# Optimization experiments

Hardware: AMD Instinct MI355X
Metric: run time of the kernel (lower is better)

## Reference

```python
import jax, jax.numpy as jnp
import numpy as np

L = 32768      # sequence length
H = 512        # n_features == d_model
P = 128        # state_size // 2 (conj_sym)
EPS = 1e-5     # haiku LayerNorm default eps


def setup_inputs() -> dict:
    key = jax.random.key(0)
    ks = jax.random.split(key, 10)
    x = jax.random.normal(ks[0], (L, H), dtype=jnp.float32)
    # S5 parameters (HiPPO-like init approximated with random values of same structure)
    lambda_real = -(0.1 + 0.5 * jax.random.uniform(ks[1], (P,), dtype=jnp.float32))
    lambda_imag = jnp.pi * jnp.arange(P, dtype=jnp.float32)
    b = jax.random.normal(ks[2], (P, H, 2), dtype=jnp.float32) / np.sqrt(H)
    c = jax.random.normal(ks[3], (H, P, 2), dtype=jnp.float32) / np.sqrt(2 * P)
    d = jax.random.normal(ks[4], (H,), dtype=jnp.float32)
    # log-uniform timescales in [1e-3, 1e-1]
    u = jax.random.uniform(ks[5], (P, 1), dtype=jnp.float32)
    delta = jnp.log(1e-3) + u * (jnp.log(1e-1) - jnp.log(1e-3))
    norm_scale = jnp.ones((H,), dtype=jnp.float32)
    norm_offset = jnp.zeros((H,), dtype=jnp.float32)
    w2 = jax.random.normal(ks[6], (H, H), dtype=jnp.float32) / np.sqrt(H)
    b2 = jnp.zeros((H,), dtype=jnp.float32)
    return {"x": x, "lambda_real": lambda_real, "lambda_imag": lambda_imag,
            "b": b, "c": c, "d": d, "delta": delta,
            "norm_scale": norm_scale, "norm_offset": norm_offset,
            "w2": w2, "b2": b2}


def _s5_block(x, lambda_real, lambda_imag, b, c, d, delta, norm_scale, norm_offset, w2, b2):
    skip = x
    # prenorm LayerNorm over last axis
    mean = jnp.mean(x, axis=-1, keepdims=True)
    var = jnp.var(x, axis=-1, keepdims=True)
    xn = (x - mean) * jax.lax.rsqrt(var + EPS) * norm_scale + norm_offset

    # --- S5 SSM ---
    lam = lambda_real + 1j * lambda_imag                      # [P]
    B = b[..., 0] + 1j * b[..., 1]                            # [P, H]
    C = c[..., 0] + 1j * c[..., 1]                            # [H, P]
    step = jnp.exp(delta[:, 0])                               # [P] (step_rescale = 1)
    # bilinear discretization
    bl = 1.0 / (1.0 - (step / 2.0) * lam)
    lam_bar = bl * (1.0 + (step / 2.0) * lam)                 # [P]
    B_bar = (bl * step)[:, None] * B                          # [P, H]

    Bu = jnp.einsum('lh,ph->lp', xn.astype(jnp.complex64), B_bar)  # [L, P]
    lam_elems = jnp.broadcast_to(lam_bar, (L, P))

    def binop(qi, qj):
        Ai, bi = qi
        Aj, bj = qj
        return Aj * Ai, Aj * bi + bj

    _, xs = jax.lax.associative_scan(binop, (lam_elems, Bu))  # states [L, P]
    # conj_sym: output is 2 * Re(C x)
    ys = 2.0 * jnp.einsum('lp,hp->lh', xs, C).real            # [L, H]
    y = ys + d * xn                                           # D skip term

    # half_glu2 (dropout_rate = 0 -> identity)
    x1 = jax.nn.gelu(y)
    out = y * jax.nn.sigmoid(x1 @ w2 + b2)
    return skip + out


def reference(x, lambda_real, lambda_imag, b, c, d, delta, norm_scale, norm_offset, w2, b2):
    return _s5_block(x, lambda_real, lambda_imag, b, c, d, delta,
                     norm_scale, norm_offset, w2, b2)
```

## Files before the change

### kernel.cpp

```cpp
#include <hip/hip_runtime.h>
#include <hip/hip_bf16.h>
#include <math.h>

#define LSEQ 32768
#define HF   512
#define PS   128
#define TWOP 256
#define NC   512
#define CL   64

typedef __attribute__((ext_vector_type(8))) short short8v;
typedef __attribute__((ext_vector_type(4))) float f32x4;

__device__ __forceinline__ float sig_fast(float z) {
    return __builtin_amdgcn_rcpf(1.0f + __expf(-z));
}
__device__ __forceinline__ float gelu_fast(float v) {
    float z = 1.5957691216057308f * v * fmaf(0.044715f, v * v, 1.0f);
    return v * sig_fast(z);
}
__device__ __forceinline__ unsigned short bf16bits(float f) {
    __hip_bfloat16 h = __float2bfloat16(f);
    return *(unsigned short*)&h;
}
__device__ __forceinline__ float bf2f(unsigned short u) {
    unsigned v = ((unsigned)u) << 16;
    return *(float*)&v;
}
__device__ __forceinline__ unsigned pk2(float a, float b) {
    return ((unsigned)bf16bits(b) << 16) | bf16bits(a);
}
__device__ __forceinline__ void gload_lds16(const void* g, void* l) {
    __builtin_amdgcn_global_load_lds(
        (const __attribute__((address_space(1))) unsigned int*)g,
        (__attribute__((address_space(3))) unsigned int*)l, 16, 0, 0);
}
__device__ __forceinline__ void wait_vm0_barrier() {
    asm volatile("s_waitcnt vmcnt(0)" ::: "memory");
    __builtin_amdgcn_s_barrier();
}

__global__ __launch_bounds__(128) void prep_lam_k(
    const float* __restrict__ lr_, const float* __restrict__ li_,
    const float* __restrict__ delta, float* lam, float* bls, float* lamPow)
{
    int p = threadIdx.x;
    float lr = lr_[p], li = li_[p];
    float step = expf(delta[p]);
    float s2 = 0.5f * step;
    float dr = 1.0f - s2 * lr, di = -s2 * li;
    float inv = 1.0f / (dr * dr + di * di);
    float blr = dr * inv, bli = -di * inv;
    float nr = 1.0f + s2 * lr, ni = s2 * li;
    float lbr = blr * nr - bli * ni;
    float lbi = blr * ni + bli * nr;
    lam[2 * p] = lbr; lam[2 * p + 1] = lbi;
    bls[2 * p] = blr * step; bls[2 * p + 1] = bli * step;
    float pr = 1.0f, pim = 0.0f;
    lamPow[2 * p] = 1.0f; lamPow[2 * p + 1] = 0.0f;
    for (int k = 1; k <= CL; k++) {
        float t = pr * lbr - pim * lbi;
        pim = pr * lbi + pim * lbr;
        pr = t;
        lamPow[k * TWOP + 2 * p] = pr;
        lamPow[k * TWOP + 2 * p + 1] = pim;
    }
}

__global__ __launch_bounds__(256) void prep_B_k(
    const float* __restrict__ b, const float* __restrict__ bls,
    unsigned short* __restrict__ bwt)
{
    int idx = blockIdx.x * 256 + threadIdx.x;
    int p = idx >> 9, h = idx & 511;
    float2 bb = *(const float2*)(b + ((size_t)p * HF + h) * 2);
    float sr = bls[2 * p], si = bls[2 * p + 1];
    bwt[(size_t)(2 * p) * HF + h]     = bf16bits(sr * bb.x - si * bb.y);
    bwt[(size_t)(2 * p + 1) * HF + h] = bf16bits(sr * bb.y + si * bb.x);
}

__global__ __launch_bounds__(256) void prep_C_k(
    const float* __restrict__ c, unsigned short* __restrict__ cwt)
{
    int idx = blockIdx.x * 256 + threadIdx.x;
    int h = idx >> 7, p = idx & 127;
    float2 cc = *(const float2*)(c + ((size_t)h * PS + p) * 2);
    *(unsigned*)(cwt + (size_t)h * TWOP + 2 * p) = pk2(2.0f * cc.x, -2.0f * cc.y);
}

__global__ __launch_bounds__(256) void prep_w2_k(
    const float* __restrict__ w2, unsigned short* __restrict__ w2t)
{
    int idx = blockIdx.x * 256 + threadIdx.x;
    int n = idx >> 9, k = idx & 511;
    w2t[(size_t)n * HF + k] = bf16bits(w2[(size_t)k * HF + n]);
}

__global__ __launch_bounds__(128) void ln_k(
    const float* __restrict__ x, const float* __restrict__ scale,
    const float* __restrict__ offs, unsigned short* __restrict__ xnbf)
{
    int row = blockIdx.x, t = threadIdx.x;
    const float4* xr = (const float4*)(x + (size_t)row * HF);
    float4 v = xr[t];
    float s = v.x + v.y + v.z + v.w;
    float q = v.x * v.x + v.y * v.y + v.z * v.z + v.w * v.w;
    #pragma unroll
    for (int off = 32; off > 0; off >>= 1) {
        s += __shfl_down(s, off);
        q += __shfl_down(q, off);
    }
    __shared__ float ss[2], qq[2];
    if ((t & 63) == 0) { ss[t >> 6] = s; qq[t >> 6] = q; }
    __syncthreads();
    float S = ss[0] + ss[1], Q = qq[0] + qq[1];
    float mean = S * (1.0f / HF);
    float var = Q * (1.0f / HF) - mean * mean;
    float rstd = rsqrtf(var + 1e-5f);
    float4 sc = ((const float4*)scale)[t];
    float4 of = ((const float4*)offs)[t];
    ushort4 hv;
    hv.x = bf16bits((v.x - mean) * rstd * sc.x + of.x);
    hv.y = bf16bits((v.y - mean) * rstd * sc.y + of.y);
    hv.z = bf16bits((v.z - mean) * rstd * sc.z + of.z);
    hv.w = bf16bits((v.w - mean) * rstd * sc.w + of.w);
    ((ushort4*)(xnbf + (size_t)row * HF))[t] = hv;
}

__global__ __launch_bounds__(256) void g1scan_k(
    const unsigned short* __restrict__ A,
    const unsigned short* __restrict__ Bt,
    unsigned short* __restrict__ xs16,
    float* __restrict__ F,
    const float* __restrict__ lam)
{
    __shared__ float yt[128 * 128];
    unsigned short* Sb = (unsigned short*)yt;
    const int K = HF;
    int flat = (blockIdx.y << 1) + blockIdx.x;
    int f2 = (flat & 7) * 64 + (flat >> 3);
    const int bxi = f2 & 1, byi = f2 >> 1;
    const int bm = byi << 7;
    const int bn = bxi << 7;
    const int tid = threadIdx.x;
    const int lane = tid & 63;
    const int wid = tid >> 6;
    const int wr = wid >> 1, wc = wid & 1;

    f32x4 acc[4][4] = {};

    const int r0 = (wid << 5) + (lane >> 2);
    const int c0 = (lane & 3) << 3;
    const unsigned short* gA = A + (size_t)(bm + r0) * K + c0;
    const unsigned short* gB = Bt + (size_t)(bn + r0) * K + c0;
    const int stA0 = (wid << 5) * 32;
    const int stA1 = ((wid << 5) + 16) * 32;
    const int aoff = ((wr << 6) + (lane & 15)) * 32 + ((lane >> 4) << 3);
    const int boff = ((wc << 6) + (lane & 15)) * 32 + ((lane >> 4) << 3);

    #define G1_STAGE(b, k0) do { \
        gload_lds16(gA + (k0), Sb + (b) * 8192 + stA0); \
        gload_lds16(gA + (k0) + (size_t)16 * K, Sb + (b) * 8192 + stA1); \
        gload_lds16(gB + (k0), Sb + (b) * 8192 + 4096 + stA0); \
        gload_lds16(gB + (k0) + (size_t)16 * K, Sb + (b) * 8192 + 4096 + stA1); \
    } while (0)
    #define G1_COMPUTE(b) do { \
        short8v a_[4], b_[4]; \
        _Pragma("unroll") \
        for (int m = 0; m < 4; m++) \
            a_[m] = *(const short8v*)(Sb + (b) * 8192 + aoff + (m << 4) * 32); \
        _Pragma("unroll") \
        for (int n = 0; n < 4; n++) \
            b_[n] = *(const short8v*)(Sb + (b) * 8192 + 4096 + boff + (n << 4) * 32); \
        _Pragma("unroll") \
        for (int m = 0; m < 4; m++) \
            _Pragma("unroll") \
            for (int n = 0; n < 4; n++) \
                acc[m][n] = __builtin_amdgcn_mfma_f32_16x16x32_bf16( \
                    a_[m], b_[n], acc[m][n], 0, 0, 0); \
    } while (0)

    G1_STAGE(0, 0);
    wait_vm0_barrier();
    #pragma unroll
    for (int t = 0; t < 16; ++t) {
        const int cur = t & 1;
        if (t + 1 < 16) G1_STAGE(cur ^ 1, (t + 1) << 5);
        G1_COMPUTE(cur);
        wait_vm0_barrier();
    }

    #pragma unroll
    for (int m = 0; m < 4; m++) {
        const int rowb = (wr << 6) + (m << 4) + ((lane >> 4) << 2);
        #pragma unroll
        for (int n = 0; n < 4; n++) {
            const int col = (wc << 6) + (n << 4) + (lane & 15);
            #pragma unroll
            for (int j = 0; j < 4; j++)
                yt[(rowb + j) * 128 + col] = acc[m][n][j];
        }
    }
    __syncthreads();

    if (tid < 128) {
        int ch = tid >> 6, q = tid & 63;
        int pg = (bxi << 6) + q;
        float lr = lam[2 * pg], liv = lam[2 * pg + 1];
        float sr = 0.0f, si = 0.0f;
        float* col = yt + (ch << 6) * 128 + 2 * q;
        #pragma unroll 8
        for (int i = 0; i < CL; i++) {
            float ur = col[i * 128], ui = col[i * 128 + 1];
            float tr = lr * sr - liv * si + ur;
            float ti = lr * si + liv * sr + ui;
            sr = tr; si = ti;
            col[i * 128] = sr; col[i * 128 + 1] = si;
        }
        int cg = (byi << 1) + ch;
        F[(size_t)cg * TWOP + (bxi << 7) + 2 * q] = sr;
        F[(size_t)cg * TWOP + (bxi << 7) + 2 * q + 1] = si;
    }
    __syncthreads();

    #pragma unroll
    for (int j = 0; j < 8; j++) {
        int fl = j * 256 + tid;
        int r = fl >> 4, ck = fl & 15;
        float4 v0 = *(float4*)&yt[r * 128 + ck * 8];
        float4 v1 = *(float4*)&yt[r * 128 + ck * 8 + 4];
        uint4 o;
        o.x = pk2(v0.x, v0.y); o.y = pk2(v0.z, v0.w);
        o.z = pk2(v1.x, v1.y); o.w = pk2(v1.z, v1.w);
        *(uint4*)(xs16 + (size_t)(bm + r) * TWOP + bn + ck * 8) = o;
    }
}

__global__ __launch_bounds__(512) void carry_k(
    const float* __restrict__ F, float* __restrict__ G,
    const float* __restrict__ lamPow)
{
    __shared__ float2 buf[NC];
    int c = threadIdx.x, p = blockIdx.x;
    float2 f = *(const float2*)(F + (size_t)c * TWOP + 2 * p);
    buf[c] = f;
    float aR = lamPow[CL * TWOP + 2 * p], aI = lamPow[CL * TWOP + 2 * p + 1];
    __syncthreads();
    #pragma unroll
    for (int d = 1; d < NC; d <<= 1) {
        bool act = (c >= d);
        float2 pv = act ? buf[c - d] : make_float2(0.0f, 0.0f);
        __syncthreads();
        if (act) {
            float2 cur = buf[c];
            cur.x += aR * pv.x - aI * pv.y;
            cur.y += aR * pv.y + aI * pv.x;
            buf[c] = cur;
        }
        __syncthreads();
        float nR = aR * aR - aI * aI;
        float nI = 2.0f * aR * aI;
        aR = nR; aI = nI;
    }
    *(float2*)(G + (size_t)c * TWOP + 2 * p) = buf[c];
}

__global__ __launch_bounds__(128) void fix_k(
    const unsigned short* __restrict__ xs16, const float* __restrict__ G,
    const float* __restrict__ lamPow, unsigned short* __restrict__ xsbf)
{
    int bc = blockIdx.x;
    int c = bc >> 2, qq = bc & 3;
    int p = threadIdx.x;
    float gr = 0.0f, gi = 0.0f;
    if (c > 0) {
        float2 g = *(const float2*)(G + (size_t)(c - 1) * TWOP + 2 * p);
        gr = g.x; gi = g.y;
    }
    size_t base = ((size_t)c * CL + (qq << 4)) * TWOP + 2 * p;
    #pragma unroll
    for (int i = 0; i < 16; i++) {
        float2 lp = *(const float2*)(lamPow + (size_t)((qq << 4) + i + 1) * TWOP + 2 * p);
        unsigned u = *(const unsigned*)(xs16 + base + (size_t)i * TWOP);
        float vr = bf2f((unsigned short)(u & 0xffff)) + lp.x * gr - lp.y * gi;
        float vi = bf2f((unsigned short)(u >> 16))    + lp.x * gi + lp.y * gr;
        *(unsigned*)(xsbf + base + (size_t)i * TWOP) = pk2(vr, vi);
    }
}

template<int MODE, int KT, int NT>
__global__ __launch_bounds__(256) void mgemm_k(
    const unsigned short* __restrict__ A, const unsigned short* __restrict__ Bt,
    const float* __restrict__ e0, const unsigned short* __restrict__ e1h,
    const float* __restrict__ e2, float* __restrict__ outF,
    unsigned short* __restrict__ o1, unsigned short* __restrict__ o2)
{
    __shared__ float smem[8192];
    unsigned short* Sb = (unsigned short*)smem;
    float* eb = smem;

    constexpr int GX = NT >> 7;
    int flat = blockIdx.y * GX + blockIdx.x;
    constexpr int NWG = GX * (LSEQ >> 7);
    int f2 = (flat & 7) * (NWG >> 3) + (flat >> 3);
    const int bm = (f2 / GX) << 7;
    const int bn = (f2 % GX) << 7;

    const int tid = threadIdx.x;
    const int lane = tid & 63;
    const int wid = tid >> 6;
    const int wr = wid >> 1, wc = wid & 1;

    f32x4 acc[4][4] = {};

    const int r0 = (wid << 5) + (lane >> 2);
    const int c0 = (lane & 3) << 3;
    const unsigned short* gA = A + (size_t)(bm + r0) * KT + c0;
    const unsigned short* gB = Bt + (size_t)(bn + r0) * KT + c0;
    const int stA0 = (wid << 5) * 32;
    const int stA1 = ((wid << 5) + 16) * 32;
    const int aoff = ((wr << 6) + (lane & 15)) * 32 + ((lane >> 4) << 3);
    const int boff = ((wc << 6) + (lane & 15)) * 32 + ((lane >> 4) << 3);
    constexpr int NSTEP = KT >> 5;

    #define MG_STAGE(b, k0) do { \
        gload_lds16(gA + (k0), Sb + (b) * 8192 + stA0); \
        gload_lds16(gA + (k0) + (size_t)16 * KT, Sb + (b) * 8192 + stA1); \
        gload_lds16(gB + (k0), Sb + (b) * 8192 + 4096 + stA0); \
        gload_lds16(gB + (k0) + (size_t)16 * KT, Sb + (b) * 8192 + 4096 + stA1); \
    } while (0)
    #define MG_COMPUTE(b) do { \
        short8v a_[4], b_[4]; \
        _Pragma("unroll") \
        for (int m = 0; m < 4; m++) \
            a_[m] = *(const short8v*)(Sb + (b) * 8192 + aoff + (m << 4) * 32); \
        _Pragma("unroll") \
        for (int n = 0; n < 4; n++) \
            b_[n] = *(const short8v*)(Sb + (b) * 8192 + 4096 + boff + (n << 4) * 32); \
        _Pragma("unroll") \
        for (int m = 0; m < 4; m++) \
            _Pragma("unroll") \
            for (int n = 0; n < 4; n++) \
                acc[m][n] = __builtin_amdgcn_mfma_f32_16x16x32_bf16( \
                    a_[m], b_[n], acc[m][n], 0, 0, 0); \
    } while (0)

    MG_STAGE(0, 0);
    wait_vm0_barrier();
    #pragma unroll
    for (int t = 0; t < NSTEP; ++t) {
        const int cur = t & 1;
        if (t + 1 < NSTEP) MG_STAGE(cur ^ 1, (t + 1) << 5);
        MG_COMPUTE(cur);
        wait_vm0_barrier();
    }

    #pragma unroll
    for (int p = 0; p < 4; p++) {
        if ((p >> 1) == wr) {
            const int mb = (p & 1) << 1;
            #pragma unroll
            for (int mm = 0; mm < 2; mm++) {
                const int lrow = (mm << 4) + ((lane >> 4) << 2);
                #pragma unroll
                for (int n = 0; n < 4; n++) {
                    const int col = (wc << 6) + (n << 4) + (lane & 15);
                    #pragma unroll
                    for (int j = 0; j < 4; j++)
                        eb[(lrow + j) * 132 + col] = acc[mb + mm][n][j];
                }
            }
        }
        __syncthreads();
        #pragma unroll
        for (int i = 0; i < 4; i++) {
            int idx = (i << 8) + tid;
            int row = idx >> 5, c4 = idx & 31;
            int gr = bm + (p << 5) + row;
            int gc = bn + (c4 << 2);
            size_t off = (size_t)gr * NT + gc;
            float4 v = *(float4*)&eb[row * 132 + (c4 << 2)];
            float4 e0v = *(const float4*)(e0 + gc);
            if (MODE == 1) {
                ushort4 xv = *(const ushort4*)(e1h + off);
                float y0 = v.x + e0v.x * bf2f(xv.x);
                float y1 = v.y + e0v.y * bf2f(xv.y);
                float y2 = v.z + e0v.z * bf2f(xv.z);
                float y3 = v.w + e0v.w * bf2f(xv.w);
                ushort4 a1, a2;
                a1.x = bf16bits(y0); a1.y = bf16bits(y1);
                a1.z = bf16bits(y2); a1.w = bf16bits(y3);
                a2.x = bf16bits(gelu_fast(y0)); a2.y = bf16bits(gelu_fast(y1));
                a2.z = bf16bits(gelu_fast(y2)); a2.w = bf16bits(gelu_fast(y3));
                *(ushort4*)(o1 + off) = a1;
                *(ushort4*)(o2 + off) = a2;
            } else {
                ushort4 yv = *(const ushort4*)(e1h + off);
                float4 xv = *(const float4*)(e2 + off);
                float4 o;
                o.x = xv.x + bf2f(yv.x) * sig_fast(v.x + e0v.x);
                o.y = xv.y + bf2f(yv.y) * sig_fast(v.y + e0v.y);
                o.z = xv.z + bf2f(yv.z) * sig_fast(v.z + e0v.z);
                o.w = xv.w + bf2f(yv.w) * sig_fast(v.w + e0v.w);
                *(float4*)(outF + off) = o;
            }
        }
        __syncthreads();
    }
}

extern "C" void kernel_launch(void* const* d_in, const int* in_sizes, int n_in,
                              void* d_out, int out_size, void* d_ws, size_t ws_size,
                              hipStream_t stream)
{
    const float* x      = (const float*)d_in[0];
    const float* lr     = (const float*)d_in[1];
    const float* li     = (const float*)d_in[2];
    const float* b      = (const float*)d_in[3];
    const float* c      = (const float*)d_in[4];
    const float* d      = (const float*)d_in[5];
    const float* delta  = (const float*)d_in[6];
    const float* nsc    = (const float*)d_in[7];
    const float* noff   = (const float*)d_in[8];
    const float* w2     = (const float*)d_in[9];
    const float* b2     = (const float*)d_in[10];
    float* out = (float*)d_out;

    unsigned short* XNBF = (unsigned short*)d_ws;
    unsigned short* YBF  = XNBF + (size_t)LSEQ * HF;
    unsigned short* XS16 = YBF + (size_t)LSEQ * HF;
    unsigned short* XSBF = XS16 + (size_t)LSEQ * TWOP;
    unsigned short* BWT  = XSBF + (size_t)LSEQ * TWOP;
    unsigned short* CWT  = BWT + (size_t)TWOP * HF;
    unsigned short* W2T  = CWT + (size_t)HF * TWOP;
    float* lam    = (float*)(W2T + (size_t)HF * HF);
    float* bls    = lam + TWOP;
    float* lamPow = bls + TWOP;
    float* F      = lamPow + (size_t)(CL + 1) * TWOP;
    float* G      = F + (size_t)NC * TWOP;

    prep_lam_k<<<1, 128, 0, stream>>>(lr, li, delta, lam, bls, lamPow);
    prep_B_k<<<(PS * HF) / 256, 256, 0, stream>>>(b, bls, BWT);
    prep_C_k<<<(HF * PS) / 256, 256, 0, stream>>>(c, CWT);
    prep_w2_k<<<(HF * HF) / 256, 256, 0, stream>>>(w2, W2T);
    ln_k<<<LSEQ, 128, 0, stream>>>(x, nsc, noff, XNBF);
    g1scan_k<<<dim3(TWOP >> 7, LSEQ >> 7), 256, 0, stream>>>(
        XNBF, BWT, XS16, F, lam);
    carry_k<<<PS, 512, 0, stream>>>(F, G, lamPow);
    fix_k<<<NC * 4, 128, 0, stream>>>(XS16, G, lamPow, XSBF);
    mgemm_k<1, TWOP, HF><<<dim3(4, LSEQ >> 7), 256, 0, stream>>>(
        XSBF, CWT, d, XNBF, nullptr, nullptr, YBF, XNBF);
    mgemm_k<2, HF, HF><<<dim3(4, LSEQ >> 7), 256, 0, stream>>>(
        XNBF, W2T, b2, YBF, x, out, nullptr, nullptr);
}
```

Measured before the change: 236.6 us.

## Merge prep kernels into one launch and widen memory accesses in LN, fix, epilogues

The four parameter-prep kernels are merged into a single launch, and the bilinear scale is recomputed per thread so the intermediate bls buffer and the dependency on it go away. LayerNorm now handles one row per wavefront with 16-byte loads and stores and drops the shared-memory reduction. The fix kernel processes 8 elements per thread with 128-bit accesses in a quarter of the blocks, and the GEMM epilogues move 8 elements per thread with wider loads and stores. The aim is to cut launch overhead and memory-instruction count in the bandwidth-bound passes, at the cost of some redundant scalar math in the prep kernel.

```diff
diff --git a/kernel.cpp b/kernel.cpp
--- a/kernel.cpp
+++ b/kernel.cpp
@@ -40,91 +40,96 @@
     __builtin_amdgcn_s_barrier();
 }
 
-__global__ __launch_bounds__(128) void prep_lam_k(
+__global__ __launch_bounds__(256) void prep_all_k(
     const float* __restrict__ lr_, const float* __restrict__ li_,
-    const float* __restrict__ delta, float* lam, float* bls, float* lamPow)
-{
-    int p = threadIdx.x;
-    float lr = lr_[p], li = li_[p];
-    float step = expf(delta[p]);
-    float s2 = 0.5f * step;
-    float dr = 1.0f - s2 * lr, di = -s2 * li;
-    float inv = 1.0f / (dr * dr + di * di);
-    float blr = dr * inv, bli = -di * inv;
-    float nr = 1.0f + s2 * lr, ni = s2 * li;
-    float lbr = blr * nr - bli * ni;
-    float lbi = blr * ni + bli * nr;
-    lam[2 * p] = lbr; lam[2 * p + 1] = lbi;
-    bls[2 * p] = blr * step; bls[2 * p + 1] = bli * step;
-    float pr = 1.0f, pim = 0.0f;
-    lamPow[2 * p] = 1.0f; lamPow[2 * p + 1] = 0.0f;
-    for (int k = 1; k <= CL; k++) {
-        float t = pr * lbr - pim * lbi;
-        pim = pr * lbi + pim * lbr;
-        pr = t;
-        lamPow[k * TWOP + 2 * p] = pr;
-        lamPow[k * TWOP + 2 * p + 1] = pim;
-    }
-}
-
-__global__ __launch_bounds__(256) void prep_B_k(
-    const float* __restrict__ b, const float* __restrict__ bls,
-    unsigned short* __restrict__ bwt)
-{
-    int idx = blockIdx.x * 256 + threadIdx.x;
-    int p = idx >> 9, h = idx & 511;
-    float2 bb = *(const float2*)(b + ((size_t)p * HF + h) * 2);
-    float sr = bls[2 * p], si = bls[2 * p + 1];
-    bwt[(size_t)(2 * p) * HF + h]     = bf16bits(sr * bb.x - si * bb.y);
-    bwt[(size_t)(2 * p + 1) * HF + h] = bf16bits(sr * bb.y + si * bb.x);
-}
-
-__global__ __launch_bounds__(256) void prep_C_k(
-    const float* __restrict__ c, unsigned short* __restrict__ cwt)
-{
-    int idx = blockIdx.x * 256 + threadIdx.x;
-    int h = idx >> 7, p = idx & 127;
-    float2 cc = *(const float2*)(c + ((size_t)h * PS + p) * 2);
-    *(unsigned*)(cwt + (size_t)h * TWOP + 2 * p) = pk2(2.0f * cc.x, -2.0f * cc.y);
-}
-
-__global__ __launch_bounds__(256) void prep_w2_k(
-    const float* __restrict__ w2, unsigned short* __restrict__ w2t)
-{
-    int idx = blockIdx.x * 256 + threadIdx.x;
-    int n = idx >> 9, k = idx & 511;
-    w2t[(size_t)n * HF + k] = bf16bits(w2[(size_t)k * HF + n]);
+    const float* __restrict__ delta, const float* __restrict__ b,
+    const float* __restrict__ c, const float* __restrict__ w2,
+    float* lam, float* lamPow,
+    unsigned short* __restrict__ bwt, unsigned short* __restrict__ cwt,
+    unsigned short* __restrict__ w2t)
+{
+    int blk = blockIdx.x, tid = threadIdx.x;
+    if (blk == 0) {
+        if (tid < 128) {
+            int p = tid;
+            float lr = lr_[p], li = li_[p];
+            float step = expf(delta[p]);
+            float s2 = 0.5f * step;
+            float dr = 1.0f - s2 * lr, di = -s2 * li;
+            float inv = 1.0f / (dr * dr + di * di);
+            float blr = dr * inv, bli = -di * inv;
+            float nr = 1.0f + s2 * lr, ni = s2 * li;
+            float lbr = blr * nr - bli * ni;
+            float lbi = blr * ni + bli * nr;
+            lam[2 * p] = lbr; lam[2 * p + 1] = lbi;
+            float pr = 1.0f, pim = 0.0f;
+            lamPow[2 * p] = 1.0f; lamPow[2 * p + 1] = 0.0f;
+            for (int k = 1; k <= CL; k++) {
+                float t = pr * lbr - pim * lbi;
+                pim = pr * lbi + pim * lbr;
+                pr = t;
+                lamPow[k * TWOP + 2 * p] = pr;
+                lamPow[k * TWOP + 2 * p + 1] = pim;
+            }
+        }
+    } else if (blk < 257) {
+        int idx = (blk - 1) * 256 + tid;
+        int p = idx >> 9, h = idx & 511;
+        float lr = lr_[p], li = li_[p];
+        float step = expf(delta[p]);
+        float s2 = 0.5f * step;
+        float dr = 1.0f - s2 * lr, di = -s2 * li;
+        float inv = 1.0f / (dr * dr + di * di);
+        float sr = dr * inv * step, si = -di * inv * step;
+        float2 bb = *(const float2*)(b + ((size_t)p * HF + h) * 2);
+        bwt[(size_t)(2 * p) * HF + h]     = bf16bits(sr * bb.x - si * bb.y);
+        bwt[(size_t)(2 * p + 1) * HF + h] = bf16bits(sr * bb.y + si * bb.x);
+    } else if (blk < 513) {
+        int idx = (blk - 257) * 256 + tid;
+        int h = idx >> 7, p = idx & 127;
+        float2 cc = *(const float2*)(c + ((size_t)h * PS + p) * 2);
+        *(unsigned*)(cwt + (size_t)h * TWOP + 2 * p) = pk2(2.0f * cc.x, -2.0f * cc.y);
+    } else {
+        int idx = (blk - 513) * 256 + tid;
+        int n = idx >> 9, k = idx & 511;
+        w2t[(size_t)n * HF + k] = bf16bits(w2[(size_t)k * HF + n]);
+    }
 }
 
 __global__ __launch_bounds__(128) void ln_k(
     const float* __restrict__ x, const float* __restrict__ scale,
     const float* __restrict__ offs, unsigned short* __restrict__ xnbf)
 {
-    int row = blockIdx.x, t = threadIdx.x;
+    int w = threadIdx.x >> 6, l = threadIdx.x & 63;
+    int row = (blockIdx.x << 1) + w;
     const float4* xr = (const float4*)(x + (size_t)row * HF);
-    float4 v = xr[t];
-    float s = v.x + v.y + v.z + v.w;
-    float q = v.x * v.x + v.y * v.y + v.z * v.z + v.w * v.w;
+    float4 a = xr[2 * l], b4 = xr[2 * l + 1];
+    float s = a.x + a.y + a.z + a.w + b4.x + b4.y + b4.z + b4.w;
+    float q = a.x * a.x + a.y * a.y + a.z * a.z + a.w * a.w
+            + b4.x * b4.x + b4.y * b4.y + b4.z * b4.z + b4.w * b4.w;
     #pragma unroll
     for (int off = 32; off > 0; off >>= 1) {
         s += __shfl_down(s, off);
         q += __shfl_down(q, off);
     }
-    __shared__ float ss[2], qq[2];
-    if ((t & 63) == 0) { ss[t >> 6] = s; qq[t >> 6] = q; }
-    __syncthreads();
-    float S = ss[0] + ss[1], Q = qq[0] + qq[1];
-    float mean = S * (1.0f / HF);
-    float var = Q * (1.0f / HF) - mean * mean;
+    s = __shfl(s, 0); q = __shfl(q, 0);
+    float mean = s * (1.0f / HF);
+    float var = q * (1.0f / HF) - mean * mean;
     float rstd = rsqrtf(var + 1e-5f);
-    float4 sc = ((const float4*)scale)[t];
-    float4 of = ((const float4*)offs)[t];
-    ushort4 hv;
-    hv.x = bf16bits((v.x - mean) * rstd * sc.x + of.x);
-    hv.y = bf16bits((v.y - mean) * rstd * sc.y + of.y);
-    hv.z = bf16bits((v.z - mean) * rstd * sc.z + of.z);
-    hv.w = bf16bits((v.w - mean) * rstd * sc.w + of.w);
-    ((ushort4*)(xnbf + (size_t)row * HF))[t] = hv;
+    float4 sc0 = ((const float4*)scale)[2 * l], sc1 = ((const float4*)scale)[2 * l + 1];
+    float4 of0 = ((const float4*)offs)[2 * l],  of1 = ((const float4*)offs)[2 * l + 1];
+    float y0 = (a.x - mean) * rstd * sc0.x + of0.x;
+    float y1 = (a.y - mean) * rstd * sc0.y + of0.y;
+    float y2 = (a.z - mean) * rstd * sc0.z + of0.z;
+    float y3 = (a.w - mean) * rstd * sc0.w + of0.w;
+    float y4 = (b4.x - mean) * rstd * sc1.x + of1.x;
+    float y5 = (b4.y - mean) * rstd * sc1.y + of1.y;
+    float y6 = (b4.z - mean) * rstd * sc1.z + of1.z;
+    float y7 = (b4.w - mean) * rstd * sc1.w + of1.w;
+    uint4 o;
+    o.x = pk2(y0, y1); o.y = pk2(y2, y3);
+    o.z = pk2(y4, y5); o.w = pk2(y6, y7);
+    *(uint4*)(xnbf + (size_t)row * HF + l * 8) = o;
 }
 
 __global__ __launch_bounds__(256) void g1scan_k(
@@ -269,22 +274,37 @@
     const unsigned short* __restrict__ xs16, const float* __restrict__ G,
     const float* __restrict__ lamPow, unsigned short* __restrict__ xsbf)
 {
-    int bc = blockIdx.x;
-    int c = bc >> 2, qq = bc & 3;
-    int p = threadIdx.x;
-    float gr = 0.0f, gi = 0.0f;
+    int c = blockIdx.x;
+    int g = threadIdx.x & 31, rsub = threadIdx.x >> 5;
+    float gr[4], gi[4];
     if (c > 0) {
-        float2 g = *(const float2*)(G + (size_t)(c - 1) * TWOP + 2 * p);
-        gr = g.x; gi = g.y;
-    }
-    size_t base = ((size_t)c * CL + (qq << 4)) * TWOP + 2 * p;
+        float4 ga = *(const float4*)(G + (size_t)(c - 1) * TWOP + g * 8);
+        float4 gb = *(const float4*)(G + (size_t)(c - 1) * TWOP + g * 8 + 4);
+        gr[0] = ga.x; gi[0] = ga.y; gr[1] = ga.z; gi[1] = ga.w;
+        gr[2] = gb.x; gi[2] = gb.y; gr[3] = gb.z; gi[3] = gb.w;
+    } else {
+        gr[0] = gr[1] = gr[2] = gr[3] = 0.0f;
+        gi[0] = gi[1] = gi[2] = gi[3] = 0.0f;
+    }
     #pragma unroll
     for (int i = 0; i < 16; i++) {
-        float2 lp = *(const float2*)(lamPow + (size_t)((qq << 4) + i + 1) * TWOP + 2 * p);
-        unsigned u = *(const unsigned*)(xs16 + base + (size_t)i * TWOP);
-        float vr = bf2f((unsigned short)(u & 0xffff)) + lp.x * gr - lp.y * gi;
-        float vi = bf2f((unsigned short)(u >> 16))    + lp.x * gi + lp.y * gr;
-        *(unsigned*)(xsbf + base + (size_t)i * TWOP) = pk2(vr, vi);
+        int row = (i << 2) + rsub;
+        size_t boff = ((size_t)c * CL + row) * TWOP + g * 8;
+        uint4 u = *(const uint4*)(xs16 + boff);
+        float4 la = *(const float4*)(lamPow + (size_t)(row + 1) * TWOP + g * 8);
+        float4 lb = *(const float4*)(lamPow + (size_t)(row + 1) * TWOP + g * 8 + 4);
+        float lpr[4] = {la.x, la.z, lb.x, lb.z};
+        float lpi[4] = {la.y, la.w, lb.y, lb.w};
+        unsigned uu[4] = {u.x, u.y, u.z, u.w};
+        uint4 o;
+        unsigned* oo = (unsigned*)&o;
+        #pragma unroll
+        for (int j = 0; j < 4; j++) {
+            float vr = bf2f((unsigned short)(uu[j] & 0xffff)) + lpr[j] * gr[j] - lpi[j] * gi[j];
+            float vi = bf2f((unsigned short)(uu[j] >> 16))    + lpr[j] * gi[j] + lpi[j] * gr[j];
+            oo[j] = pk2(vr, vi);
+        }
+        *(uint4*)(xsbf + boff) = o;
     }
 }
 
@@ -373,36 +393,51 @@
         }
         __syncthreads();
         #pragma unroll
-        for (int i = 0; i < 4; i++) {
+        for (int i = 0; i < 2; i++) {
             int idx = (i << 8) + tid;
-            int row = idx >> 5, c4 = idx & 31;
+            int row = idx >> 4, cp = idx & 15;
             int gr = bm + (p << 5) + row;
-            int gc = bn + (c4 << 2);
+            int gc = bn + (cp << 3);
             size_t off = (size_t)gr * NT + gc;
-            float4 v = *(float4*)&eb[row * 132 + (c4 << 2)];
-            float4 e0v = *(const float4*)(e0 + gc);
+            float4 v0 = *(float4*)&eb[row * 132 + (cp << 3)];
+            float4 v1 = *(float4*)&eb[row * 132 + (cp << 3) + 4];
+            float4 e0a = *(const float4*)(e0 + gc);
+            float4 e0b = *(const float4*)(e0 + gc + 4);
+            uint4 hv = *(const uint4*)(e1h + off);
+            const unsigned* hh = (const unsigned*)&hv;
+            float ev[8] = {e0a.x, e0a.y, e0a.z, e0a.w, e0b.x, e0b.y, e0b.z, e0b.w};
+            float av[8] = {v0.x, v0.y, v0.z, v0.w, v1.x, v1.y, v1.z, v1.w};
             if (MODE == 1) {
-                ushort4 xv = *(const ushort4*)(e1h + off);
-                float y0 = v.x + e0v.x * bf2f(xv.x);
-                float y1 = v.y + e0v.y * bf2f(xv.y);
-                float y2 = v.z + e0v.z * bf2f(xv.z);
-                float y3 = v.w + e0v.w * bf2f(xv.w);
-                ushort4 a1, a2;
-                a1.x = bf16bits(y0); a1.y = bf16bits(y1);
-                a1.z = bf16bits(y2); a1.w = bf16bits(y3);
-                a2.x = bf16bits(gelu_fast(y0)); a2.y = bf16bits(gelu_fast(y1));
-                a2.z = bf16bits(gelu_fast(y2)); a2.w = bf16bits(gelu_fast(y3));
-                *(ushort4*)(o1 + off) = a1;
-                *(ushort4*)(o2 + off) = a2;
+                float y[8];
+                #pragma unroll
+                for (int j = 0; j < 8; j++) {
+                    unsigned short xb = (j & 1) ? (unsigned short)(hh[j >> 1] >> 16)
+                                                : (unsigned short)(hh[j >> 1] & 0xffff);
+                    y[j] = av[j] + ev[j] * bf2f(xb);
+                }
+                uint4 a1, a2;
+                unsigned* p1 = (unsigned*)&a1;
+                unsigned* p2 = (unsigned*)&a2;
+                #pragma unroll
+                for (int j = 0; j < 4; j++) {
+                    p1[j] = pk2(y[2 * j], y[2 * j + 1]);
+                    p2[j] = pk2(gelu_fast(y[2 * j]), gelu_fast(y[2 * j + 1]));
+                }
+                *(uint4*)(o1 + off) = a1;
+                *(uint4*)(o2 + off) = a2;
             } else {
-                ushort4 yv = *(const ushort4*)(e1h + off);
-                float4 xv = *(const float4*)(e2 + off);
-                float4 o;
-                o.x = xv.x + bf2f(yv.x) * sig_fast(v.x + e0v.x);
-                o.y = xv.y + bf2f(yv.y) * sig_fast(v.y + e0v.y);
-                o.z = xv.z + bf2f(yv.z) * sig_fast(v.z + e0v.z);
-                o.w = xv.w + bf2f(yv.w) * sig_fast(v.w + e0v.w);
-                *(float4*)(outF + off) = o;
+                float4 x0 = *(const float4*)(e2 + off);
+                float4 x1 = *(const float4*)(e2 + off + 4);
+                float xv[8] = {x0.x, x0.y, x0.z, x0.w, x1.x, x1.y, x1.z, x1.w};
+                float o[8];
+                #pragma unroll
+                for (int j = 0; j < 8; j++) {
+                    unsigned short yb = (j & 1) ? (unsigned short)(hh[j >> 1] >> 16)
+                                                : (unsigned short)(hh[j >> 1] & 0xffff);
+                    o[j] = xv[j] + bf2f(yb) * sig_fast(av[j] + ev[j]);
+                }
+                *(float4*)(outF + off)     = make_float4(o[0], o[1], o[2], o[3]);
+                *(float4*)(outF + off + 4) = make_float4(o[4], o[5], o[6], o[7]);
             }
         }
         __syncthreads();
@@ -434,20 +469,17 @@
     unsigned short* CWT  = BWT + (size_t)TWOP * HF;
     unsigned short* W2T  = CWT + (size_t)HF * TWOP;
     float* lam    = (float*)(W2T + (size_t)HF * HF);
-    float* bls    = lam + TWOP;
-    float* lamPow = bls + TWOP;
+    float* lamPow = lam + TWOP;
     float* F      = lamPow + (size_t)(CL + 1) * TWOP;
     float* G      = F + (size_t)NC * TWOP;
 
-    prep_lam_k<<<1, 128, 0, stream>>>(lr, li, delta, lam, bls, lamPow);
-    prep_B_k<<<(PS * HF) / 256, 256, 0, stream>>>(b, bls, BWT);
-    prep_C_k<<<(HF * PS) / 256, 256, 0, stream>>>(c, CWT);
-    prep_w2_k<<<(HF * HF) / 256, 256, 0, stream>>>(w2, W2T);
-    ln_k<<<LSEQ, 128, 0, stream>>>(x, nsc, noff, XNBF);
+    prep_all_k<<<1537, 256, 0, stream>>>(lr, li, delta, b, c, w2,
+                                         lam, lamPow, BWT, CWT, W2T);
+    ln_k<<<LSEQ / 2, 128, 0, stream>>>(x, nsc, noff, XNBF);
     g1scan_k<<<dim3(TWOP >> 7, LSEQ >> 7), 256, 0, stream>>>(
         XNBF, BWT, XS16, F, lam);
     carry_k<<<PS, 512, 0, stream>>>(F, G, lamPow);
-    fix_k<<<NC * 4, 128, 0, stream>>>(XS16, G, lamPow, XSBF);
+    fix_k<<<NC, 128, 0, stream>>>(XS16, G, lamPow, XSBF);
     mgemm_k<1, TWOP, HF><<<dim3(4, LSEQ >> 7), 256, 0, stream>>>(
         XSBF, CWT, d, XNBF, nullptr, nullptr, YBF, XNBF);
     mgemm_k<2, HF, HF><<<dim3(4, LSEQ >> 7), 256, 0, stream>>>(
```

After: 225.4 us. 1.05x faster.
